# Kernel tuning notes

Hardware: AMD Instinct MI355X
Metric: run time of the kernel (lower is better)

## Reference

```python
import jax, jax.numpy as jnp
import numpy as np

N = 100000   # nodes
E = 50000    # hyperedges
K = 4        # nodes per hyperedge
D = 128      # out_dim (= in_dim here)
ED = 64      # edge_dim
H = 8        # num_heads


def _build_pairs(seed=0):
    # Sparse equivalent of the incidence-matrix nested loops:
    # for each edge e with member set S, emit ordered pairs (v, e, u) for v,u in S.
    rng = np.random.default_rng(seed)
    cover = rng.permutation(N).reshape(N // K, K)          # guarantees every node owns >=1 pair group
    rand = rng.integers(0, N, size=(E - N // K, K))
    edge_nodes = np.concatenate([cover, rand], axis=0)      # [E, K]
    owners = np.repeat(edge_nodes, K, axis=1).ravel()       # v, repeated K times per edge slot
    pair_u = np.tile(edge_nodes, (1, K)).ravel()            # u, tiled
    pair_e = np.repeat(np.arange(E), K * K)
    return owners.astype(np.int32), pair_e.astype(np.int32), pair_u.astype(np.int32)


def setup_inputs() -> dict:
    key = jax.random.key(0)
    ks = jax.random.split(key, 12)
    owners, pair_e, pair_u = _build_pairs()
    s = 0.05
    return {
        "x": jax.random.normal(ks[0], (N, D), jnp.float32),
        "edge_attr": jax.random.normal(ks[1], (E, ED), jnp.float32),
        "w_lin": jax.random.normal(ks[2], (D, D), jnp.float32) * s,   # self.lin (no bias)
        "w_e": jax.random.normal(ks[3], (ED, D), jnp.float32) * s,    # self.edge_lin (no bias)
        "w_q": jax.random.normal(ks[4], (D, D), jnp.float32) * s,
        "b_q": jax.random.normal(ks[5], (D,), jnp.float32) * s,
        "w_k": jax.random.normal(ks[6], (D, D), jnp.float32) * s,
        "b_k": jax.random.normal(ks[7], (D,), jnp.float32) * s,
        "w_v": jax.random.normal(ks[8], (D, D), jnp.float32) * s,
        "b_v": jax.random.normal(ks[9], (D,), jnp.float32) * s,
        "w_o": jax.random.normal(ks[10], (D, D), jnp.float32) * s,
        "b_o": jax.random.normal(ks[11], (D,), jnp.float32) * s,
        "owners": jnp.asarray(owners),
        "pair_e": jnp.asarray(pair_e),
        "pair_u": jnp.asarray(pair_u),
    }


def reference(x, edge_attr, w_lin, w_e, w_q, b_q, w_k, b_k, w_v, b_v, w_o, b_o, owners, pair_e, pair_u):
    n = x.shape[0]
    d = w_lin.shape[1]
    dh = d // H
    Wh = x @ w_lin                                  # [N, D]
    We = edge_attr @ w_e                            # [E, D]
    # Multi-head single-query attention per node over its (e,u) pair set.
    q = ((Wh @ w_q + b_q) / jnp.sqrt(jnp.asarray(dh, Wh.dtype))).reshape(n, H, dh)
    Wh_u = Wh[pair_u]                               # [P, D] value source (= Wh[u])
    k = ((Wh_u + We[pair_e]) @ w_k + b_k).reshape(-1, H, dh)   # key source = Wh[u] + We[e]
    v = (Wh_u @ w_v + b_v).reshape(-1, H, dh)
    scores = jnp.einsum('phd,phd->ph', q[owners], k)            # [P, H]
    # segmented (ragged) softmax over each node's pair set
    m = jax.ops.segment_max(scores, owners, num_segments=n)
    ex = jnp.exp(scores - m[owners])
    denom = jax.ops.segment_sum(ex, owners, num_segments=n)     # [N, H]
    alpha = ex / denom[owners]                                  # [P, H]
    ctx = jax.ops.segment_sum(alpha[..., None] * v, owners, num_segments=n).reshape(n, d)
    out = ctx @ w_o + b_o
    return jax.nn.relu(out)
```

## Files before the change

kernel.cpp:

```cpp
#include <hip/hip_runtime.h>

#define NN 100000
#define EE 50000
#define GG (EE*4)
#define NB 391

typedef __attribute__((ext_vector_type(8))) short bf16x8;
typedef __attribute__((ext_vector_type(4))) float f32x4;

__device__ __forceinline__ unsigned short f2bf(float f) {
  union { float f; unsigned int u; } c; c.f = f;
  unsigned int u = c.u;
  u = (u + 0x7fffu + ((u >> 16) & 1u)) >> 16;
  return (unsigned short)u;
}
__device__ __forceinline__ float bf2f(unsigned int lo16) {
  union { unsigned int u; float f; } c; c.u = lo16 << 16;
  return c.f;
}
__device__ __forceinline__ bf16x8 pack8(const float* f) {
  union { bf16x8 v; unsigned int u[4]; } r;
  #pragma unroll
  for (int i = 0; i < 4; ++i)
    r.u[i] = (unsigned int)f2bf(f[2*i]) | ((unsigned int)f2bf(f[2*i+1]) << 16);
  return r.v;
}

struct __align__(8) us4 { unsigned short x, y, z, w; };

__global__ void k_prep(const float* __restrict__ w_lin, const float* __restrict__ w_e,
                       const float* __restrict__ w_q, const float* __restrict__ b_q,
                       const float* __restrict__ w_k, const float* __restrict__ b_k,
                       const float* __restrict__ w_v, const float* __restrict__ b_v,
                       const float* __restrict__ w_o, const float* __restrict__ b_o,
                       unsigned short* __restrict__ WT, unsigned short* __restrict__ WeT,
                       unsigned short* __restrict__ WoT, float* __restrict__ bias384,
                       float* __restrict__ bkB, float* __restrict__ boB) {
  int t = blockIdx.x * 256 + threadIdx.x;
  if (t < 49152) {
    int n = t >> 7, k = t & 127;
    const float* wsel; int nn; float scale = 1.0f;
    if (n < 128)      { wsel = w_q; nn = n;       scale = 0.25f; }
    else if (n < 256) { wsel = w_k; nn = n - 128; }
    else              { wsel = w_v; nn = n - 256; }
    float s = 0.f;
    for (int d = 0; d < 128; ++d) s += w_lin[k*128 + d] * wsel[d*128 + nn];
    WT[n*128 + k] = f2bf(s * scale);
  } else if (t < 57344) {
    int i = t - 49152, n = i >> 6, k = i & 63;
    float s = 0.f;
    for (int d = 0; d < 128; ++d) s += w_e[k*128 + d] * w_k[d*128 + n];
    WeT[n*64 + k] = f2bf(s);
  } else if (t < 73728) {
    int i = t - 57344, n = i >> 7, k = i & 127;
    WoT[n*128 + k] = f2bf(w_o[k*128 + n]);
  } else if (t < 74112) {
    int i = t - 73728;
    bias384[i] = (i < 128) ? b_q[i] * 0.25f : ((i < 256) ? 0.f : b_v[i - 256]);
  } else if (t < 74240) {
    bkB[t - 74112] = b_k[t - 74112];
  } else if (t < 74368) {
    boB[t - 74240] = b_o[t - 74240];
  }
}

__global__ __launch_bounds__(256) void k_qkv(const float* __restrict__ x,
                                             const unsigned short* __restrict__ WT,
                                             const float* __restrict__ bias,
                                             unsigned short* __restrict__ qkv) {
  __shared__ unsigned short As[64 * 136];
  int tid = threadIdx.x;
  int row0 = blockIdx.x * 64;
  #pragma unroll
  for (int it = 0; it < 8; ++it) {
    int i4 = tid + it * 256;
    int r = i4 >> 5, c4 = i4 & 31;
    float4 vv = make_float4(0.f, 0.f, 0.f, 0.f);
    int gr = row0 + r;
    if (gr < NN) vv = *(const float4*)(x + (size_t)gr * 128 + c4 * 4);
    us4 s4 = { f2bf(vv.x), f2bf(vv.y), f2bf(vv.z), f2bf(vv.w) };
    int chunk = c4 >> 1;
    int soff = r * 128 + ((chunk ^ (r & 7)) << 3) + ((c4 & 1) << 2);
    *(us4*)(&As[soff]) = s4;
  }
  __syncthreads();
  int w = tid >> 6, lane = tid & 63, lr = lane & 15, lk = lane >> 4;
  bf16x8 afr[4][4];
  #pragma unroll
  for (int rt = 0; rt < 4; ++rt) {
    int R = rt * 16 + lr;
    #pragma unroll
    for (int kk = 0; kk < 4; ++kk) {
      int chunk = (kk * 4 + lk) ^ (R & 7);
      afr[rt][kk] = *(const bf16x8*)(&As[R * 128 + chunk * 8]);
    }
  }
  #pragma unroll
  for (int p = 0; p < 3; ++p) {
    f32x4 acc[2][4] = {};
    #pragma unroll
    for (int h = 0; h < 2; ++h) {
      int gcol = p * 128 + h * 64 + w * 16 + lr;
      const unsigned short* bp = WT + (size_t)gcol * 128 + lk * 8;
      bf16x8 b0 = *(const bf16x8*)(bp);
      bf16x8 b1 = *(const bf16x8*)(bp + 32);
      bf16x8 b2 = *(const bf16x8*)(bp + 64);
      bf16x8 b3 = *(const bf16x8*)(bp + 96);
      #pragma unroll
      for (int rt = 0; rt < 4; ++rt) {
        acc[h][rt] = __builtin_amdgcn_mfma_f32_16x16x32_bf16(afr[rt][0], b0, acc[h][rt], 0, 0, 0);
        acc[h][rt] = __builtin_amdgcn_mfma_f32_16x16x32_bf16(afr[rt][1], b1, acc[h][rt], 0, 0, 0);
        acc[h][rt] = __builtin_amdgcn_mfma_f32_16x16x32_bf16(afr[rt][2], b2, acc[h][rt], 0, 0, 0);
        acc[h][rt] = __builtin_amdgcn_mfma_f32_16x16x32_bf16(afr[rt][3], b3, acc[h][rt], 0, 0, 0);
      }
    }
    __syncthreads();
    #pragma unroll
    for (int h = 0; h < 2; ++h) {
      int colp = h * 64 + w * 16 + lr;
      float b = bias[p * 128 + colp];
      #pragma unroll
      for (int rt = 0; rt < 4; ++rt) {
        #pragma unroll
        for (int j = 0; j < 4; ++j) {
          As[(rt * 16 + lk * 4 + j) * 136 + colp] = f2bf(acc[h][rt][j] + b);
        }
      }
    }
    __syncthreads();
    int piece = tid & 15, rbase = tid >> 4;
    #pragma unroll
    for (int it = 0; it < 4; ++it) {
      int r = rbase + it * 16;
      int grow = row0 + r;
      if (grow < NN) {
        float4 vv = *(const float4*)(&As[r * 136 + piece * 8]);
        *(float4*)(qkv + (size_t)grow * 384 + p * 128 + piece * 8) = vv;
      }
    }
  }
}

__global__ __launch_bounds__(256) void k_ke(const float* __restrict__ ea,
                                            const unsigned short* __restrict__ WeT,
                                            const float* __restrict__ bk,
                                            unsigned short* __restrict__ ke) {
  __shared__ unsigned short As[64][72];
  __shared__ unsigned short Bs[64][72];
  int tid = threadIdx.x;
  int row0 = blockIdx.x * 64;
  int col0 = blockIdx.y * 64;
  #pragma unroll
  for (int it = 0; it < 4; ++it) {
    int i4 = tid + it * 256;
    int r = i4 >> 4, c4 = i4 & 15;
    float4 vv = make_float4(0.f, 0.f, 0.f, 0.f);
    int gr = row0 + r;
    if (gr < EE) vv = *(const float4*)(ea + (size_t)gr * 64 + c4 * 4);
    us4 s4 = { f2bf(vv.x), f2bf(vv.y), f2bf(vv.z), f2bf(vv.w) };
    *(us4*)(&As[r][c4 * 4]) = s4;
  }
  #pragma unroll
  for (int it = 0; it < 4; ++it) {
    int i4 = tid + it * 256;
    int r = i4 >> 4, c4 = i4 & 15;
    us4 s4 = *(const us4*)(WeT + (size_t)(col0 + r) * 64 + c4 * 4);
    *(us4*)(&Bs[r][c4 * 4]) = s4;
  }
  __syncthreads();
  int w = tid >> 6, lane = tid & 63, lr = lane & 15, lk = lane >> 4;
  f32x4 acc[4] = {};
  #pragma unroll
  for (int kk = 0; kk < 2; ++kk) {
    int kof = kk * 32 + lk * 8;
    bf16x8 af = *(const bf16x8*)(&As[w * 16 + lr][kof]);
    #pragma unroll
    for (int nt = 0; nt < 4; ++nt) {
      bf16x8 bfrag = *(const bf16x8*)(&Bs[nt * 16 + lr][kof]);
      acc[nt] = __builtin_amdgcn_mfma_f32_16x16x32_bf16(af, bfrag, acc[nt], 0, 0, 0);
    }
  }
  #pragma unroll
  for (int nt = 0; nt < 4; ++nt) {
    int gcol = col0 + nt * 16 + lr;
    float b = bk[gcol];
    #pragma unroll
    for (int j = 0; j < 4; ++j) {
      int grow = row0 + w * 16 + lk * 4 + j;
      if (grow < EE) ke[(size_t)grow * 128 + gcol] = f2bf(acc[nt][j] + b);
    }
  }
}

__global__ void k_count(const int* __restrict__ owners, int* __restrict__ counts) {
  int g = blockIdx.x * 256 + threadIdx.x;
  if (g < GG) atomicAdd(counts + owners[(size_t)g * 4], 1);
}

__global__ __launch_bounds__(256) void k_scan1(const int* __restrict__ counts,
                                               int* __restrict__ lofs,
                                               int* __restrict__ bsums) {
  __shared__ int tmp[256];
  int tid = threadIdx.x;
  int i = blockIdx.x * 256 + tid;
  int v = (i < NN) ? counts[i] : 0;
  tmp[tid] = v;
  __syncthreads();
  int val = v;
  #pragma unroll
  for (int off = 1; off < 256; off <<= 1) {
    int t = (tid >= off) ? tmp[tid - off] : 0;
    __syncthreads();
    val += t;
    tmp[tid] = val;
    __syncthreads();
  }
  if (i < NN) lofs[i] = val - v;
  if (tid == 255) bsums[blockIdx.x] = val;
}

__global__ __launch_bounds__(512) void k_scan2(int* __restrict__ bsums) {
  __shared__ int tmp[512];
  int tid = threadIdx.x;
  int v = (tid < NB) ? bsums[tid] : 0;
  tmp[tid] = v;
  __syncthreads();
  int val = v;
  #pragma unroll
  for (int off = 1; off < 512; off <<= 1) {
    int t = (tid >= off) ? tmp[tid - off] : 0;
    __syncthreads();
    val += t;
    tmp[tid] = val;
    __syncthreads();
  }
  if (tid < NB) bsums[tid] = val - v;
}

__global__ void k_scan3(const int* __restrict__ lofs, const int* __restrict__ bsums,
                        int* __restrict__ starts, int* __restrict__ wcursor) {
  int i = blockIdx.x * 256 + threadIdx.x;
  if (i < NN) {
    int s = lofs[i] + bsums[i >> 8];
    starts[i] = s;
    wcursor[i] = s;
  }
  if (i == 0) starts[NN] = GG;
}

__global__ void k_scatter(const int* __restrict__ owners, int* __restrict__ wcursor,
                          int* __restrict__ pos) {
  int g = blockIdx.x * 256 + threadIdx.x;
  if (g < GG) {
    int v = owners[(size_t)g * 4];
    pos[g] = atomicAdd(wcursor + v, 1);
  }
}

__global__ __launch_bounds__(256) void k_edge(const unsigned short* __restrict__ qkv,
                                              const unsigned short* __restrict__ ke,
                                              const int* __restrict__ pair_u,
                                              const int* __restrict__ pos,
                                              unsigned short* __restrict__ pctx,
                                              float* __restrict__ pden) {
  int e0 = (blockIdx.x * 4 + (threadIdx.x >> 6)) * 2;
  if (e0 >= EE) return;
  int lane = threadIdx.x & 63;
  int m[2][4], ps[2][4];
  #pragma unroll
  for (int ee = 0; ee < 2; ++ee)
    #pragma unroll
    for (int j = 0; j < 4; ++j) {
      m[ee][j]  = __builtin_amdgcn_readfirstlane(pair_u[(size_t)(e0 + ee) * 16 + j]);
      ps[ee][j] = __builtin_amdgcn_readfirstlane(pos[(size_t)(e0 + ee) * 4 + j]);
    }
  float ev[2][2];
  #pragma unroll
  for (int ee = 0; ee < 2; ++ee) {
    unsigned int kew = *(const unsigned int*)(ke + (size_t)(e0 + ee) * 128 + 2 * lane);
    ev[ee][0] = bf2f(kew & 0xffffu); ev[ee][1] = bf2f(kew >> 16);
  }
  float qa[2][4][2], ka[2][4][2], va[2][4][2];
  #pragma unroll
  for (int ee = 0; ee < 2; ++ee)
    #pragma unroll
    for (int j = 0; j < 4; ++j) {
      const unsigned short* r = qkv + (size_t)m[ee][j] * 384 + 2 * lane;
      unsigned int qw = *(const unsigned int*)r;
      unsigned int kw = *(const unsigned int*)(r + 128);
      unsigned int vw = *(const unsigned int*)(r + 256);
      qa[ee][j][0] = bf2f(qw & 0xffffu);             qa[ee][j][1] = bf2f(qw >> 16);
      ka[ee][j][0] = bf2f(kw & 0xffffu) + ev[ee][0]; ka[ee][j][1] = bf2f(kw >> 16) + ev[ee][1];
      va[ee][j][0] = bf2f(vw & 0xffffu);             va[ee][j][1] = bf2f(vw >> 16);
    }
  #pragma unroll
  for (int ee = 0; ee < 2; ++ee)
    #pragma unroll
    for (int i = 0; i < 4; ++i) {
      float c0 = 0.f, c1 = 0.f, ds = 0.f;
      #pragma unroll
      for (int j = 0; j < 4; ++j) {
        float sc = qa[ee][i][0] * ka[ee][j][0] + qa[ee][i][1] * ka[ee][j][1];
        sc += __shfl_xor(sc, 1);
        sc += __shfl_xor(sc, 2);
        sc += __shfl_xor(sc, 4);
        float ex = __expf(sc);
        c0 += ex * va[ee][j][0];
        c1 += ex * va[ee][j][1];
        ds += ex;
      }
      unsigned int packed = (unsigned int)f2bf(c0) | ((unsigned int)f2bf(c1) << 16);
      *(unsigned int*)(pctx + (size_t)ps[ee][i] * 128 + 2 * lane) = packed;
      if ((lane & 7) == 0) pden[(size_t)ps[ee][i] * 8 + (lane >> 3)] = ds;
    }
}

__global__ __launch_bounds__(256) void k_out(const unsigned short* __restrict__ pctx,
                                             const float* __restrict__ pden,
                                             const int* __restrict__ starts,
                                             const unsigned short* __restrict__ WoT,
                                             const float* __restrict__ bo,
                                             float* __restrict__ out) {
  int wid = blockIdx.x * 4 + (threadIdx.x >> 6);
  if (wid >= NN / 16) return;
  int lane = threadIdx.x & 63, lr = lane & 15, lk = lane >> 4;
  int row = wid * 16 + lr;
  float a[4][8];
  float ds[4] = { 0.f, 0.f, 0.f, 0.f };
  #pragma unroll
  for (int kk = 0; kk < 4; ++kk)
    #pragma unroll
    for (int i = 0; i < 8; ++i) a[kk][i] = 0.f;
  int s0 = starts[row], s1 = starts[row + 1];
  for (int sl = s0; sl < s1; ++sl) {
    const unsigned short* pr = pctx + (size_t)sl * 128 + lk * 8;
    const float* dp = pden + (size_t)sl * 8 + (lk >> 1);
    #pragma unroll
    for (int kk = 0; kk < 4; ++kk) {
      uint4 v = *(const uint4*)(pr + kk * 32);
      a[kk][0] += bf2f(v.x & 0xffffu); a[kk][1] += bf2f(v.x >> 16);
      a[kk][2] += bf2f(v.y & 0xffffu); a[kk][3] += bf2f(v.y >> 16);
      a[kk][4] += bf2f(v.z & 0xffffu); a[kk][5] += bf2f(v.z >> 16);
      a[kk][6] += bf2f(v.w & 0xffffu); a[kk][7] += bf2f(v.w >> 16);
      ds[kk] += dp[kk * 2];
    }
  }
  bf16x8 abf[4];
  #pragma unroll
  for (int kk = 0; kk < 4; ++kk) {
    float inv = ds[kk] > 0.f ? 1.0f / ds[kk] : 0.f;
    float f[8];
    #pragma unroll
    for (int i = 0; i < 8; ++i) f[i] = a[kk][i] * inv;
    abf[kk] = pack8(f);
  }
  #pragma unroll
  for (int ct = 0; ct < 8; ++ct) {
    const unsigned short* wp = WoT + (size_t)(ct * 16 + lr) * 128 + lk * 8;
    bf16x8 w0 = *(const bf16x8*)(wp);
    bf16x8 w1 = *(const bf16x8*)(wp + 32);
    bf16x8 w2 = *(const bf16x8*)(wp + 64);
    bf16x8 w3 = *(const bf16x8*)(wp + 96);
    f32x4 acc = {};
    acc = __builtin_amdgcn_mfma_f32_16x16x32_bf16(w0, abf[0], acc, 0, 0, 0);
    acc = __builtin_amdgcn_mfma_f32_16x16x32_bf16(w1, abf[1], acc, 0, 0, 0);
    acc = __builtin_amdgcn_mfma_f32_16x16x32_bf16(w2, abf[2], acc, 0, 0, 0);
    acc = __builtin_amdgcn_mfma_f32_16x16x32_bf16(w3, abf[3], acc, 0, 0, 0);
    float4 bb = *(const float4*)(bo + ct * 16 + lk * 4);
    float4 o;
    o.x = fmaxf(acc[0] + bb.x, 0.f);
    o.y = fmaxf(acc[1] + bb.y, 0.f);
    o.z = fmaxf(acc[2] + bb.z, 0.f);
    o.w = fmaxf(acc[3] + bb.w, 0.f);
    *(float4*)(out + (size_t)row * 128 + ct * 16 + lk * 4) = o;
  }
}

extern "C" void kernel_launch(void* const* d_in, const int* in_sizes, int n_in,
                              void* d_out, int out_size, void* d_ws, size_t ws_size,
                              hipStream_t stream) {
  const float* x      = (const float*)d_in[0];
  const float* ea     = (const float*)d_in[1];
  const float* w_lin  = (const float*)d_in[2];
  const float* w_e    = (const float*)d_in[3];
  const float* w_q    = (const float*)d_in[4];
  const float* b_q    = (const float*)d_in[5];
  const float* w_k    = (const float*)d_in[6];
  const float* b_k    = (const float*)d_in[7];
  const float* w_v    = (const float*)d_in[8];
  const float* b_v    = (const float*)d_in[9];
  const float* w_o    = (const float*)d_in[10];
  const float* b_o    = (const float*)d_in[11];
  const int* owners   = (const int*)d_in[12];
  const int* pair_u   = (const int*)d_in[14];
  float* out = (float*)d_out;

  char* base = (char*)d_ws;
  size_t o = 0;
  auto alloc = [&](size_t b) {
    void* p = base + o;
    o = (o + b + 255) & ~(size_t)255;
    return p;
  };
  unsigned short* WT      = (unsigned short*)alloc((size_t)384 * 128 * 2);
  unsigned short* WeT     = (unsigned short*)alloc((size_t)128 * 64 * 2);
  unsigned short* WoT     = (unsigned short*)alloc((size_t)128 * 128 * 2);
  float* bias384          = (float*)alloc(384 * 4);
  float* bkB              = (float*)alloc(128 * 4);
  float* boB              = (float*)alloc(128 * 4);
  unsigned short* qkv     = (unsigned short*)alloc((size_t)NN * 384 * 2);
  unsigned short* keb     = (unsigned short*)alloc((size_t)EE * 128 * 2);
  int* counts             = (int*)alloc((size_t)NN * 4);
  int* starts             = (int*)alloc((size_t)(NN + 1) * 4);
  int* wcursor            = (int*)alloc((size_t)NN * 4);
  int* pos                = (int*)alloc((size_t)GG * 4);
  int* lofs               = (int*)alloc((size_t)NN * 4);
  int* bsums              = (int*)alloc((size_t)NB * 4);
  unsigned short* pctx    = (unsigned short*)alloc((size_t)GG * 128 * 2);
  float* pden             = (float*)alloc((size_t)GG * 8 * 4);

  hipMemsetAsync(counts, 0, (size_t)NN * 4, stream);

  k_prep<<<291, 256, 0, stream>>>(w_lin, w_e, w_q, b_q, w_k, b_k, w_v, b_v, w_o, b_o,
                                  WT, WeT, WoT, bias384, bkB, boB);
  k_qkv<<<1563, 256, 0, stream>>>(x, WT, bias384, qkv);
  k_ke<<<dim3(782, 2), 256, 0, stream>>>(ea, WeT, bkB, keb);
  k_count<<<782, 256, 0, stream>>>(owners, counts);
  k_scan1<<<NB, 256, 0, stream>>>(counts, lofs, bsums);
  k_scan2<<<1, 512, 0, stream>>>(bsums);
  k_scan3<<<NB, 256, 0, stream>>>(lofs, bsums, starts, wcursor);
  k_scatter<<<782, 256, 0, stream>>>(owners, wcursor, pos);
  k_edge<<<6250, 256, 0, stream>>>(qkv, keb, pair_u, pos, pctx, pden);
  k_out<<<1563, 256, 0, stream>>>(pctx, pden, starts, WoT, boB, out);
}
```

Before: 178.8 us.

## Split QKV GEMM across grid, batch more edges per wave, two row-tiles in output kernel

k_qkv now launches a 3-wide grid in y so each block computes one 128-column slice (q, k or v), instead of looping over all three. This removes the serial per-block loop and its barriers, but each block re-reads and re-converts its x tile three times. k_edge processes four hyperedges per wave instead of two, issuing all gathers up front to get more loads in flight, at the cost of more registers. k_out handles 32 rows per wave with interleaved ragged accumulation for two 16-row tiles, sharing the W_o fragment loads. That adds register pressure and divergence from uneven segment lengths.

```diff
diff --git a/kernel.cpp b/kernel.cpp
--- a/kernel.cpp
+++ b/kernel.cpp
@@ -71,6 +71,7 @@
   __shared__ unsigned short As[64 * 136];
   int tid = threadIdx.x;
   int row0 = blockIdx.x * 64;
+  int col0 = blockIdx.y * 128;
   #pragma unroll
   for (int it = 0; it < 8; ++it) {
     int i4 = tid + it * 256;
@@ -95,48 +96,45 @@
       afr[rt][kk] = *(const bf16x8*)(&As[R * 128 + chunk * 8]);
     }
   }
-  #pragma unroll
-  for (int p = 0; p < 3; ++p) {
-    f32x4 acc[2][4] = {};
-    #pragma unroll
-    for (int h = 0; h < 2; ++h) {
-      int gcol = p * 128 + h * 64 + w * 16 + lr;
-      const unsigned short* bp = WT + (size_t)gcol * 128 + lk * 8;
-      bf16x8 b0 = *(const bf16x8*)(bp);
-      bf16x8 b1 = *(const bf16x8*)(bp + 32);
-      bf16x8 b2 = *(const bf16x8*)(bp + 64);
-      bf16x8 b3 = *(const bf16x8*)(bp + 96);
+  f32x4 acc[2][4] = {};
+  #pragma unroll
+  for (int h = 0; h < 2; ++h) {
+    int gcol = col0 + h * 64 + w * 16 + lr;
+    const unsigned short* bp = WT + (size_t)gcol * 128 + lk * 8;
+    bf16x8 b0 = *(const bf16x8*)(bp);
+    bf16x8 b1 = *(const bf16x8*)(bp + 32);
+    bf16x8 b2 = *(const bf16x8*)(bp + 64);
+    bf16x8 b3 = *(const bf16x8*)(bp + 96);
+    #pragma unroll
+    for (int rt = 0; rt < 4; ++rt) {
+      acc[h][rt] = __builtin_amdgcn_mfma_f32_16x16x32_bf16(afr[rt][0], b0, acc[h][rt], 0, 0, 0);
+      acc[h][rt] = __builtin_amdgcn_mfma_f32_16x16x32_bf16(afr[rt][1], b1, acc[h][rt], 0, 0, 0);
+      acc[h][rt] = __builtin_amdgcn_mfma_f32_16x16x32_bf16(afr[rt][2], b2, acc[h][rt], 0, 0, 0);
+      acc[h][rt] = __builtin_amdgcn_mfma_f32_16x16x32_bf16(afr[rt][3], b3, acc[h][rt], 0, 0, 0);
+    }
+  }
+  __syncthreads();
+  #pragma unroll
+  for (int h = 0; h < 2; ++h) {
+    int colp = h * 64 + w * 16 + lr;
+    float b = bias[col0 + colp];
+    #pragma unroll
+    for (int rt = 0; rt < 4; ++rt) {
       #pragma unroll
-      for (int rt = 0; rt < 4; ++rt) {
-        acc[h][rt] = __builtin_amdgcn_mfma_f32_16x16x32_bf16(afr[rt][0], b0, acc[h][rt], 0, 0, 0);
-        acc[h][rt] = __builtin_amdgcn_mfma_f32_16x16x32_bf16(afr[rt][1], b1, acc[h][rt], 0, 0, 0);
-        acc[h][rt] = __builtin_amdgcn_mfma_f32_16x16x32_bf16(afr[rt][2], b2, acc[h][rt], 0, 0, 0);
-        acc[h][rt] = __builtin_amdgcn_mfma_f32_16x16x32_bf16(afr[rt][3], b3, acc[h][rt], 0, 0, 0);
+      for (int j = 0; j < 4; ++j) {
+        As[(rt * 16 + lk * 4 + j) * 136 + colp] = f2bf(acc[h][rt][j] + b);
       }
     }
-    __syncthreads();
-    #pragma unroll
-    for (int h = 0; h < 2; ++h) {
-      int colp = h * 64 + w * 16 + lr;
-      float b = bias[p * 128 + colp];
-      #pragma unroll
-      for (int rt = 0; rt < 4; ++rt) {
-        #pragma unroll
-        for (int j = 0; j < 4; ++j) {
-          As[(rt * 16 + lk * 4 + j) * 136 + colp] = f2bf(acc[h][rt][j] + b);
-        }
-      }
-    }
-    __syncthreads();
-    int piece = tid & 15, rbase = tid >> 4;
-    #pragma unroll
-    for (int it = 0; it < 4; ++it) {
-      int r = rbase + it * 16;
-      int grow = row0 + r;
-      if (grow < NN) {
-        float4 vv = *(const float4*)(&As[r * 136 + piece * 8]);
-        *(float4*)(qkv + (size_t)grow * 384 + p * 128 + piece * 8) = vv;
-      }
+  }
+  __syncthreads();
+  int piece = tid & 15, rbase = tid >> 4;
+  #pragma unroll
+  for (int it = 0; it < 4; ++it) {
+    int r = rbase + it * 16;
+    int grow = row0 + r;
+    if (grow < NN) {
+      float4 vv = *(const float4*)(&As[r * 136 + piece * 8]);
+      *(float4*)(qkv + (size_t)grow * 384 + col0 + piece * 8) = vv;
     }
   }
 }
@@ -263,56 +261,60 @@
                                               const int* __restrict__ pos,
                                               unsigned short* __restrict__ pctx,
                                               float* __restrict__ pden) {
-  int e0 = (blockIdx.x * 4 + (threadIdx.x >> 6)) * 2;
+  int e0 = (blockIdx.x * 4 + (threadIdx.x >> 6)) * 4;
   if (e0 >= EE) return;
   int lane = threadIdx.x & 63;
-  int m[2][4], ps[2][4];
-  #pragma unroll
-  for (int ee = 0; ee < 2; ++ee)
+  int m[4][4], ps[4][4];
+  #pragma unroll
+  for (int ee = 0; ee < 4; ++ee)
     #pragma unroll
     for (int j = 0; j < 4; ++j) {
       m[ee][j]  = __builtin_amdgcn_readfirstlane(pair_u[(size_t)(e0 + ee) * 16 + j]);
       ps[ee][j] = __builtin_amdgcn_readfirstlane(pos[(size_t)(e0 + ee) * 4 + j]);
     }
-  float ev[2][2];
-  #pragma unroll
-  for (int ee = 0; ee < 2; ++ee) {
-    unsigned int kew = *(const unsigned int*)(ke + (size_t)(e0 + ee) * 128 + 2 * lane);
-    ev[ee][0] = bf2f(kew & 0xffffu); ev[ee][1] = bf2f(kew >> 16);
-  }
-  float qa[2][4][2], ka[2][4][2], va[2][4][2];
-  #pragma unroll
-  for (int ee = 0; ee < 2; ++ee)
+  unsigned int kew[4];
+  #pragma unroll
+  for (int ee = 0; ee < 4; ++ee)
+    kew[ee] = *(const unsigned int*)(ke + (size_t)(e0 + ee) * 128 + 2 * lane);
+  unsigned int qw[4][4], kw[4][4], vw[4][4];
+  #pragma unroll
+  for (int ee = 0; ee < 4; ++ee)
     #pragma unroll
     for (int j = 0; j < 4; ++j) {
       const unsigned short* r = qkv + (size_t)m[ee][j] * 384 + 2 * lane;
-      unsigned int qw = *(const unsigned int*)r;
-      unsigned int kw = *(const unsigned int*)(r + 128);
-      unsigned int vw = *(const unsigned int*)(r + 256);
-      qa[ee][j][0] = bf2f(qw & 0xffffu);             qa[ee][j][1] = bf2f(qw >> 16);
-      ka[ee][j][0] = bf2f(kw & 0xffffu) + ev[ee][0]; ka[ee][j][1] = bf2f(kw >> 16) + ev[ee][1];
-      va[ee][j][0] = bf2f(vw & 0xffffu);             va[ee][j][1] = bf2f(vw >> 16);
-    }
-  #pragma unroll
-  for (int ee = 0; ee < 2; ++ee)
+      qw[ee][j] = *(const unsigned int*)r;
+      kw[ee][j] = *(const unsigned int*)(r + 128);
+      vw[ee][j] = *(const unsigned int*)(r + 256);
+    }
+  #pragma unroll
+  for (int ee = 0; ee < 4; ++ee) {
+    float e0f = bf2f(kew[ee] & 0xffffu), e1f = bf2f(kew[ee] >> 16);
+    float qa[4][2], ka[4][2], va[4][2];
+    #pragma unroll
+    for (int j = 0; j < 4; ++j) {
+      qa[j][0] = bf2f(qw[ee][j] & 0xffffu);        qa[j][1] = bf2f(qw[ee][j] >> 16);
+      ka[j][0] = bf2f(kw[ee][j] & 0xffffu) + e0f;  ka[j][1] = bf2f(kw[ee][j] >> 16) + e1f;
+      va[j][0] = bf2f(vw[ee][j] & 0xffffu);        va[j][1] = bf2f(vw[ee][j] >> 16);
+    }
     #pragma unroll
     for (int i = 0; i < 4; ++i) {
       float c0 = 0.f, c1 = 0.f, ds = 0.f;
       #pragma unroll
       for (int j = 0; j < 4; ++j) {
-        float sc = qa[ee][i][0] * ka[ee][j][0] + qa[ee][i][1] * ka[ee][j][1];
+        float sc = qa[i][0] * ka[j][0] + qa[i][1] * ka[j][1];
         sc += __shfl_xor(sc, 1);
         sc += __shfl_xor(sc, 2);
         sc += __shfl_xor(sc, 4);
         float ex = __expf(sc);
-        c0 += ex * va[ee][j][0];
-        c1 += ex * va[ee][j][1];
+        c0 += ex * va[j][0];
+        c1 += ex * va[j][1];
         ds += ex;
       }
       unsigned int packed = (unsigned int)f2bf(c0) | ((unsigned int)f2bf(c1) << 16);
       *(unsigned int*)(pctx + (size_t)ps[ee][i] * 128 + 2 * lane) = packed;
       if ((lane & 7) == 0) pden[(size_t)ps[ee][i] * 8 + (lane >> 3)] = ds;
     }
+  }
 }
 
 __global__ __launch_bounds__(256) void k_out(const unsigned short* __restrict__ pctx,
@@ -322,37 +324,59 @@
                                              const float* __restrict__ bo,
                                              float* __restrict__ out) {
   int wid = blockIdx.x * 4 + (threadIdx.x >> 6);
-  if (wid >= NN / 16) return;
+  if (wid >= NN / 32) return;
   int lane = threadIdx.x & 63, lr = lane & 15, lk = lane >> 4;
-  int row = wid * 16 + lr;
-  float a[4][8];
-  float ds[4] = { 0.f, 0.f, 0.f, 0.f };
+  int rowA = wid * 32 + lr, rowB = rowA + 16;
+  float aA[4][8], aB[4][8];
+  float dsA[4] = { 0.f, 0.f, 0.f, 0.f }, dsB[4] = { 0.f, 0.f, 0.f, 0.f };
   #pragma unroll
   for (int kk = 0; kk < 4; ++kk)
     #pragma unroll
-    for (int i = 0; i < 8; ++i) a[kk][i] = 0.f;
-  int s0 = starts[row], s1 = starts[row + 1];
-  for (int sl = s0; sl < s1; ++sl) {
-    const unsigned short* pr = pctx + (size_t)sl * 128 + lk * 8;
-    const float* dp = pden + (size_t)sl * 8 + (lk >> 1);
-    #pragma unroll
-    for (int kk = 0; kk < 4; ++kk) {
-      uint4 v = *(const uint4*)(pr + kk * 32);
-      a[kk][0] += bf2f(v.x & 0xffffu); a[kk][1] += bf2f(v.x >> 16);
-      a[kk][2] += bf2f(v.y & 0xffffu); a[kk][3] += bf2f(v.y >> 16);
-      a[kk][4] += bf2f(v.z & 0xffffu); a[kk][5] += bf2f(v.z >> 16);
-      a[kk][6] += bf2f(v.w & 0xffffu); a[kk][7] += bf2f(v.w >> 16);
-      ds[kk] += dp[kk * 2];
-    }
-  }
-  bf16x8 abf[4];
+    for (int i = 0; i < 8; ++i) { aA[kk][i] = 0.f; aB[kk][i] = 0.f; }
+  int slA = starts[rowA], eA = starts[rowA + 1];
+  int slB = starts[rowB], eB = starts[rowB + 1];
+  for (;;) {
+    bool doA = slA < eA, doB = slB < eB;
+    if (!__any((int)(doA || doB))) break;
+    if (doA) {
+      const unsigned short* pr = pctx + (size_t)slA * 128 + lk * 8;
+      const float* dp = pden + (size_t)slA * 8 + (lk >> 1);
+      #pragma unroll
+      for (int kk = 0; kk < 4; ++kk) {
+        uint4 v = *(const uint4*)(pr + kk * 32);
+        aA[kk][0] += bf2f(v.x & 0xffffu); aA[kk][1] += bf2f(v.x >> 16);
+        aA[kk][2] += bf2f(v.y & 0xffffu); aA[kk][3] += bf2f(v.y >> 16);
+        aA[kk][4] += bf2f(v.z & 0xffffu); aA[kk][5] += bf2f(v.z >> 16);
+        aA[kk][6] += bf2f(v.w & 0xffffu); aA[kk][7] += bf2f(v.w >> 16);
+        dsA[kk] += dp[kk * 2];
+      }
+      ++slA;
+    }
+    if (doB) {
+      const unsigned short* pr = pctx + (size_t)slB * 128 + lk * 8;
+      const float* dp = pden + (size_t)slB * 8 + (lk >> 1);
+      #pragma unroll
+      for (int kk = 0; kk < 4; ++kk) {
+        uint4 v = *(const uint4*)(pr + kk * 32);
+        aB[kk][0] += bf2f(v.x & 0xffffu); aB[kk][1] += bf2f(v.x >> 16);
+        aB[kk][2] += bf2f(v.y & 0xffffu); aB[kk][3] += bf2f(v.y >> 16);
+        aB[kk][4] += bf2f(v.z & 0xffffu); aB[kk][5] += bf2f(v.z >> 16);
+        aB[kk][6] += bf2f(v.w & 0xffffu); aB[kk][7] += bf2f(v.w >> 16);
+        dsB[kk] += dp[kk * 2];
+      }
+      ++slB;
+    }
+  }
+  bf16x8 abfA[4], abfB[4];
   #pragma unroll
   for (int kk = 0; kk < 4; ++kk) {
-    float inv = ds[kk] > 0.f ? 1.0f / ds[kk] : 0.f;
-    float f[8];
-    #pragma unroll
-    for (int i = 0; i < 8; ++i) f[i] = a[kk][i] * inv;
-    abf[kk] = pack8(f);
+    float invA = dsA[kk] > 0.f ? 1.0f / dsA[kk] : 0.f;
+    float invB = dsB[kk] > 0.f ? 1.0f / dsB[kk] : 0.f;
+    float fA[8], fB[8];
+    #pragma unroll
+    for (int i = 0; i < 8; ++i) { fA[i] = aA[kk][i] * invA; fB[i] = aB[kk][i] * invB; }
+    abfA[kk] = pack8(fA);
+    abfB[kk] = pack8(fB);
   }
   #pragma unroll
   for (int ct = 0; ct < 8; ++ct) {
@@ -361,18 +385,23 @@
     bf16x8 w1 = *(const bf16x8*)(wp + 32);
     bf16x8 w2 = *(const bf16x8*)(wp + 64);
     bf16x8 w3 = *(const bf16x8*)(wp + 96);
-    f32x4 acc = {};
-    acc = __builtin_amdgcn_mfma_f32_16x16x32_bf16(w0, abf[0], acc, 0, 0, 0);
-    acc = __builtin_amdgcn_mfma_f32_16x16x32_bf16(w1, abf[1], acc, 0, 0, 0);
-    acc = __builtin_amdgcn_mfma_f32_16x16x32_bf16(w2, abf[2], acc, 0, 0, 0);
-    acc = __builtin_amdgcn_mfma_f32_16x16x32_bf16(w3, abf[3], acc, 0, 0, 0);
+    f32x4 accA = {}, accB = {};
+    accA = __builtin_amdgcn_mfma_f32_16x16x32_bf16(w0, abfA[0], accA, 0, 0, 0);
+    accA = __builtin_amdgcn_mfma_f32_16x16x32_bf16(w1, abfA[1], accA, 0, 0, 0);
+    accA = __builtin_amdgcn_mfma_f32_16x16x32_bf16(w2, abfA[2], accA, 0, 0, 0);
+    accA = __builtin_amdgcn_mfma_f32_16x16x32_bf16(w3, abfA[3], accA, 0, 0, 0);
+    accB = __builtin_amdgcn_mfma_f32_16x16x32_bf16(w0, abfB[0], accB, 0, 0, 0);
+    accB = __builtin_amdgcn_mfma_f32_16x16x32_bf16(w1, abfB[1], accB, 0, 0, 0);
+    accB = __builtin_amdgcn_mfma_f32_16x16x32_bf16(w2, abfB[2], accB, 0, 0, 0);
+    accB = __builtin_amdgcn_mfma_f32_16x16x32_bf16(w3, abfB[3], accB, 0, 0, 0);
     float4 bb = *(const float4*)(bo + ct * 16 + lk * 4);
-    float4 o;
-    o.x = fmaxf(acc[0] + bb.x, 0.f);
-    o.y = fmaxf(acc[1] + bb.y, 0.f);
-    o.z = fmaxf(acc[2] + bb.z, 0.f);
-    o.w = fmaxf(acc[3] + bb.w, 0.f);
-    *(float4*)(out + (size_t)row * 128 + ct * 16 + lk * 4) = o;
+    float4 oA, oB;
+    oA.x = fmaxf(accA[0] + bb.x, 0.f); oA.y = fmaxf(accA[1] + bb.y, 0.f);
+    oA.z = fmaxf(accA[2] + bb.z, 0.f); oA.w = fmaxf(accA[3] + bb.w, 0.f);
+    oB.x = fmaxf(accB[0] + bb.x, 0.f); oB.y = fmaxf(accB[1] + bb.y, 0.f);
+    oB.z = fmaxf(accB[2] + bb.z, 0.f); oB.w = fmaxf(accB[3] + bb.w, 0.f);
+    *(float4*)(out + (size_t)rowA * 128 + ct * 16 + lk * 4) = oA;
+    *(float4*)(out + (size_t)rowB * 128 + ct * 16 + lk * 4) = oB;
   }
 }
 
@@ -423,13 +452,13 @@
 
   k_prep<<<291, 256, 0, stream>>>(w_lin, w_e, w_q, b_q, w_k, b_k, w_v, b_v, w_o, b_o,
                                   WT, WeT, WoT, bias384, bkB, boB);
-  k_qkv<<<1563, 256, 0, stream>>>(x, WT, bias384, qkv);
+  k_qkv<<<dim3(1563, 3), 256, 0, stream>>>(x, WT, bias384, qkv);
   k_ke<<<dim3(782, 2), 256, 0, stream>>>(ea, WeT, bkB, keb);
   k_count<<<782, 256, 0, stream>>>(owners, counts);
   k_scan1<<<NB, 256, 0, stream>>>(counts, lofs, bsums);
   k_scan2<<<1, 512, 0, stream>>>(bsums);
   k_scan3<<<NB, 256, 0, stream>>>(lofs, bsums, starts, wcursor);
   k_scatter<<<782, 256, 0, stream>>>(owners, wcursor, pos);
-  k_edge<<<6250, 256, 0, stream>>>(qkv, keb, pair_u, pos, pctx, pden);
-  k_out<<<1563, 256, 0, stream>>>(pctx, pden, starts, WoT, boB, out);
-}
+  k_edge<<<3125, 256, 0, stream>>>(qkv, keb, pair_u, pos, pctx, pden);
+  k_out<<<782, 256, 0, stream>>>(pctx, pden, starts, WoT, boB, out);
+}
```

New measurement: 177.8 us. No clear change (-0.6%).
